# Optimization experiments

Measured on AMD Instinct MI355X. Metric: run time of the kernel, lower is better.

The kernel has to match this reference:

```python
import jax, jax.numpy as jnp
import numpy as np

B, N, NUM = 16384, 512, 3  # batch, num queries, num vanishing points per image


def setup_inputs() -> dict:
    key = jax.random.key(0)
    k1, k2, k3 = jax.random.split(key, 3)
    pred_logits = jax.random.normal(k1, (B, N, 1), jnp.float32)
    pp = jax.random.normal(k2, (B, N, 3), jnp.float32)
    pred_pos = pp / jnp.linalg.norm(pp, axis=-1, keepdims=True)  # unit directions
    vp = jax.random.normal(k3, (B, 3, NUM), jnp.float32)
    vps_unique = vp / jnp.linalg.norm(vp, axis=1, keepdims=True)  # all columns valid (abs-sum > 1e-5)
    return {"pred_logits": pred_logits, "pred_pos": pred_pos, "vps_unique": vps_unique}


def _greedy_select(conf, pos, num):
    # conf: [N,1], pos: [N,3]; greedy angular NMS keeping `num` candidates.
    order = jnp.argsort(-conf[:, 0]).astype(jnp.int32)  # descending confidence
    thresh = jnp.pi / (num + 1)
    ar = jnp.arange(num)
    cand0 = jnp.zeros((num,), jnp.int32).at[0].set(order[0])

    def step(carry, idx):
        cand, count = carry
        sel = pos[cand]                                   # [num,3]
        dots = jnp.minimum(jnp.abs(sel @ pos[idx]), 1.0)  # clip for arccos stability
        ang = jnp.where(ar < count, jnp.arccos(dots), jnp.inf)
        add = (count < num) & (jnp.min(ang) >= thresh)    # torch: skip if dst < pi/(num+1)
        cand = jnp.where(add & (ar == count), idx, cand)
        return (cand, count + add.astype(jnp.int32)), None

    (cand, _), _ = jax.lax.scan(step, (cand0, jnp.int32(1)), order[1:])
    return pos[cand]  # [num,3]


def reference(pred_logits, pred_pos, vps_unique):
    num = vps_unique.shape[2]  # static: all vps columns are valid by construction
    sel = jax.vmap(lambda c, p: _greedy_select(c, p, num))(pred_logits, pred_pos)
    return sel  # [B, num, 3]
```

## Files before the change

### kernel.cpp

```cpp
#include <hip/hip_runtime.h>
#include <math.h>

#define B_TOTAL 16384
#define NQ 512
#define NUM 3
#define TOPK 8

__global__ __launch_bounds__(256) void greedy_nms_kernel(
    const float* __restrict__ conf,
    const float* __restrict__ pos,
    float* __restrict__ out)
{
    const int lane = threadIdx.x & 63;
    const int b = (blockIdx.x << 2) | (threadIdx.x >> 6);

    const float* cb = conf + (size_t)b * NQ;
    const float* pb = pos  + (size_t)b * NQ * 3;

    const float4* cb4 = reinterpret_cast<const float4*>(cb);
    float4 c0 = cb4[lane * 2 + 0];
    float4 c1 = cb4[lane * 2 + 1];
    const float p0x = pb[0], p0y = pb[1], p0z = pb[2];

    unsigned k[8];
    {
        float f[8] = {c0.x, c0.y, c0.z, c0.w, c1.x, c1.y, c1.z, c1.w};
        #pragma unroll
        for (int s = 0; s < 8; ++s) {
            int bi = __float_as_int(f[s]);
            k[s] = (unsigned)bi ^ ((unsigned)(bi >> 31) | 0x80000000u);
        }
    }

    auto argmax64 = [&]() -> unsigned long long {
        bool s01 = k[1] > k[0];
        unsigned m01 = s01 ? k[1] : k[0]; int i01 = s01 ? 1 : 0;
        bool s23 = k[3] > k[2];
        unsigned m23 = s23 ? k[3] : k[2]; int i23 = s23 ? 3 : 2;
        bool s45 = k[5] > k[4];
        unsigned m45 = s45 ? k[5] : k[4]; int i45 = s45 ? 5 : 4;
        bool s67 = k[7] > k[6];
        unsigned m67 = s67 ? k[7] : k[6]; int i67 = s67 ? 7 : 6;
        if (m23 > m01) { m01 = m23; i01 = i23; }
        if (m67 > m45) { m45 = m67; i45 = i67; }
        if (m45 > m01) { m01 = m45; i01 = i45; }
        unsigned long long key =
            ((unsigned long long)m01 << 32) |
            (unsigned)(NQ - 1 - ((lane << 3) + i01));
        #pragma unroll
        for (int off = 1; off < 64; off <<= 1) {
            unsigned long long o = __shfl_xor(key, off);
            if (o > key) key = o;
        }
        return key;
    };

    auto consume = [&](int n) {
        const int osl = ((n >> 3) == lane) ? (n & 7) : 8;
        #pragma unroll
        for (int s = 0; s < 8; ++s)
            if (osl == s) k[s] = 0u;
    };

    int myw = 0;
    #pragma unroll
    for (int i = 0; i < TOPK; ++i) {
        unsigned long long K = argmax64();
        const int n = NQ - 1 - (int)(K & 0x1ffu);
        if (lane == i) myw = n;
        consume(n);
    }

    float cx = pb[myw * 3 + 0];
    float cy = pb[myw * 3 + 1];
    float cz = pb[myw * 3 + 2];

    const float TH  = 0.78539816339744830961f;
    const float CLO = 0.70710478f;
    const float CHI = 0.70710878f;

    auto pass1 = [&](float ax, float ay, float az,
                     float px, float py, float pz) -> bool {
        float d = fabsf(ax * px + ay * py + az * pz);
        if (d <= CLO) return true;
        if (d >= CHI) return false;
        return acosf(fminf(d, 1.f)) >= TH;
    };

    const float p1x = __shfl(cx, 0), p1y = __shfl(cy, 0), p1z = __shfl(cz, 0);
    unsigned long long ball1 =
        __ballot(pass1(p1x, p1y, p1z, cx, cy, cz)) & 0xFEull;

    float o2x = p0x, o2y = p0y, o2z = p0z;
    float o3x = p0x, o3y = p0y, o3z = p0z;
    bool need_fallback;
    float a1x = 0.f, a1y = 0.f, a1z = 0.f;
    int count = 1;

    if (ball1 != 0) {
        const int i2 = __ffsll(ball1) - 1;
        const float p2x = __shfl(cx, i2), p2y = __shfl(cy, i2),
                    p2z = __shfl(cz, i2);
        o2x = p2x; o2y = p2y; o2z = p2z;
        a1x = p2x; a1y = p2y; a1z = p2z;
        count = 2;
        unsigned long long ball3 =
            ball1 & __ballot(pass1(p2x, p2y, p2z, cx, cy, cz))
                  & ~((2ull << i2) - 1);
        if (ball3 != 0) {
            const int i3 = __ffsll(ball3) - 1;
            o3x = __shfl(cx, i3); o3y = __shfl(cy, i3); o3z = __shfl(cz, i3);
            need_fallback = false;
        } else {
            need_fallback = true;
        }
    } else {
        need_fallback = true;
    }

    if (need_fallback) {
        #pragma unroll 1
        for (int it = TOPK; it < NQ; ++it) {
            unsigned long long K = argmax64();
            if ((unsigned)(K >> 32) == 0u) break;
            const int n = NQ - 1 - (int)(K & 0x1ffu);
            consume(n);
            const float px = pb[n * 3 + 0];
            const float py = pb[n * 3 + 1];
            const float pz = pb[n * 3 + 2];
            bool add = pass1(p1x, p1y, p1z, px, py, pz) &&
                       pass1(a1x, a1y, a1z, px, py, pz);
            if (add) {
                if (count == 1) {
                    o2x = px; o2y = py; o2z = pz;
                    a1x = px; a1y = py; a1z = pz;
                    count = 2;
                } else {
                    o3x = px; o3y = py; o3z = pz;
                    break;
                }
            }
        }
    }

    if (lane == 0) {
        float* ob = out + (size_t)b * 9;
        ob[0] = p1x; ob[1] = p1y; ob[2] = p1z;
        ob[3] = o2x; ob[4] = o2y; ob[5] = o2z;
        ob[6] = o3x; ob[7] = o3y; ob[8] = o3z;
    }
}

extern "C" void kernel_launch(void* const* d_in, const int* in_sizes, int n_in,
                              void* d_out, int out_size, void* d_ws, size_t ws_size,
                              hipStream_t stream) {
    const float* pred_logits = (const float*)d_in[0];
    const float* pred_pos    = (const float*)d_in[1];
    float* out = (float*)d_out;

    const int grid = B_TOTAL / 4;
    greedy_nms_kernel<<<grid, 256, 0, stream>>>(pred_logits, pred_pos, out);
}
```

Before: 32.52 us.

## Replace iterative top-8 argmax with bitonic-merge top-8 across the wavefront

Each lane sorts its 8 packed (score, index) keys with a sorting network. Six xor-shuffle stages then merge pairs of sorted 8-lists, keeping the top 8, so every lane holds the wavefront's global top 8. This replaces eight sequential 64-lane argmax reductions, each with 6 dependent shuffles, with 6 stages of 8 parallel 64-bit shuffles and compare-swaps. The common case then exits early after the two ballot tests, and the sequential fallback runs only when the top 8 does not yield three picks. In exchange it uses more registers and issues more shuffle instructions in total.

```diff
diff --git a/kernel.cpp b/kernel.cpp
--- a/kernel.cpp
+++ b/kernel.cpp
@@ -4,7 +4,8 @@
 #define B_TOTAL 16384
 #define NQ 512
 #define NUM 3
-#define TOPK 8
+
+typedef unsigned long long u64;
 
 __global__ __launch_bounds__(256) void greedy_nms_kernel(
     const float* __restrict__ conf,
@@ -20,19 +21,118 @@
     const float4* cb4 = reinterpret_cast<const float4*>(cb);
     float4 c0 = cb4[lane * 2 + 0];
     float4 c1 = cb4[lane * 2 + 1];
+
+    u64 s[8];
+    {
+        float f[8] = {c0.x, c0.y, c0.z, c0.w, c1.x, c1.y, c1.z, c1.w};
+        #pragma unroll
+        for (int i = 0; i < 8; ++i) {
+            int bi = __float_as_int(f[i]);
+            unsigned u = (unsigned)bi ^ ((unsigned)(bi >> 31) | 0x80000000u);
+            s[i] = ((u64)u << 32) | (unsigned)(NQ - 1 - ((lane << 3) + i));
+        }
+    }
+
+    #define CSW(a, c) { if ((c) > (a)) { u64 t_ = (a); (a) = (c); (c) = t_; } }
+
+    CSW(s[0],s[1]) CSW(s[2],s[3]) CSW(s[4],s[5]) CSW(s[6],s[7])
+    CSW(s[0],s[2]) CSW(s[1],s[3]) CSW(s[4],s[6]) CSW(s[5],s[7])
+    CSW(s[1],s[2]) CSW(s[5],s[6])
+    CSW(s[0],s[4]) CSW(s[1],s[5]) CSW(s[2],s[6]) CSW(s[3],s[7])
+    CSW(s[2],s[4]) CSW(s[3],s[5])
+    CSW(s[1],s[2]) CSW(s[3],s[4]) CSW(s[5],s[6])
+
+    #pragma unroll
+    for (int off = 1; off < 64; off <<= 1) {
+        u64 o[8];
+        #pragma unroll
+        for (int i = 0; i < 8; ++i) o[i] = __shfl_xor(s[i], off);
+        u64 m[8];
+        #pragma unroll
+        for (int i = 0; i < 8; ++i) {
+            u64 x = o[7 - i];
+            m[i] = s[i] > x ? s[i] : x;
+        }
+        CSW(m[0],m[4]) CSW(m[1],m[5]) CSW(m[2],m[6]) CSW(m[3],m[7])
+        CSW(m[0],m[2]) CSW(m[1],m[3]) CSW(m[4],m[6]) CSW(m[5],m[7])
+        CSW(m[0],m[1]) CSW(m[2],m[3]) CSW(m[4],m[5]) CSW(m[6],m[7])
+        #pragma unroll
+        for (int i = 0; i < 8; ++i) s[i] = m[i];
+    }
+
+    int myn = NQ - 1 - (int)(s[0] & 0x1ffu);
+    #pragma unroll
+    for (int i = 1; i < 8; ++i)
+        if (lane == i) myn = NQ - 1 - (int)(s[i] & 0x1ffu);
+    float cx = pb[myn * 3 + 0];
+    float cy = pb[myn * 3 + 1];
+    float cz = pb[myn * 3 + 2];
+
+    const float TH  = 0.78539816339744830961f;
+    const float CLO = 0.70710478f;
+    const float CHI = 0.70710878f;
+
+    auto passv = [&](float ax, float ay, float az,
+                     float px, float py, float pz) -> bool {
+        float d = fabsf(ax * px + ay * py + az * pz);
+        if (d <= CLO) return true;
+        if (d >= CHI) return false;
+        return acosf(fminf(d, 1.f)) >= TH;
+    };
+
+    const float p1x = __shfl(cx, 0), p1y = __shfl(cy, 0), p1z = __shfl(cz, 0);
+    u64 ball1 = __ballot(passv(p1x, p1y, p1z, cx, cy, cz)) & 0xFEull;
+
+    float o2x, o2y, o2z;
+    const bool found2 = (ball1 != 0);
+    if (found2) {
+        const int i2 = __ffsll(ball1) - 1;
+        o2x = __shfl(cx, i2); o2y = __shfl(cy, i2); o2z = __shfl(cz, i2);
+        u64 ball3 = ball1 & __ballot(passv(o2x, o2y, o2z, cx, cy, cz))
+                          & ~((2ull << i2) - 1);
+        if (ball3 != 0) {
+            const int i3 = __ffsll(ball3) - 1;
+            const float o3x = __shfl(cx, i3);
+            const float o3y = __shfl(cy, i3);
+            const float o3z = __shfl(cz, i3);
+            if (lane == 0) {
+                float* ob = out + (size_t)b * 9;
+                ob[0] = p1x; ob[1] = p1y; ob[2] = p1z;
+                ob[3] = o2x; ob[4] = o2y; ob[5] = o2z;
+                ob[6] = o3x; ob[7] = o3y; ob[8] = o3z;
+            }
+            return;
+        }
+    }
+
     const float p0x = pb[0], p0y = pb[1], p0z = pb[2];
 
     unsigned k[8];
     {
         float f[8] = {c0.x, c0.y, c0.z, c0.w, c1.x, c1.y, c1.z, c1.w};
         #pragma unroll
-        for (int s = 0; s < 8; ++s) {
-            int bi = __float_as_int(f[s]);
-            k[s] = (unsigned)bi ^ ((unsigned)(bi >> 31) | 0x80000000u);
+        for (int i = 0; i < 8; ++i) {
+            int bi = __float_as_int(f[i]);
+            k[i] = (unsigned)bi ^ ((unsigned)(bi >> 31) | 0x80000000u);
         }
     }
+    #pragma unroll
+    for (int r = 0; r < 8; ++r) {
+        const int nr = NQ - 1 - (int)(s[r] & 0x1ffu);
+        const int osl = ((nr >> 3) == lane) ? (nr & 7) : 8;
+        #pragma unroll
+        for (int q = 0; q < 8; ++q)
+            if (osl == q) k[q] = 0u;
+    }
 
-    auto argmax64 = [&]() -> unsigned long long {
+    float a1x = 0.f, a1y = 0.f, a1z = 0.f;
+    float o3x = p0x, o3y = p0y, o3z = p0z;
+    int count;
+    if (found2) { a1x = o2x; a1y = o2y; a1z = o2z; count = 2; }
+    else        { o2x = p0x; o2y = p0y; o2z = p0z; count = 1; }
+
+    #pragma unroll 1
+    for (int it = 8; it < NQ; ++it) {
         bool s01 = k[1] > k[0];
         unsigned m01 = s01 ? k[1] : k[0]; int i01 = s01 ? 1 : 0;
         bool s23 = k[3] > k[2];
@@ -44,101 +144,34 @@
         if (m23 > m01) { m01 = m23; i01 = i23; }
         if (m67 > m45) { m45 = m67; i45 = i67; }
         if (m45 > m01) { m01 = m45; i01 = i45; }
-        unsigned long long key =
-            ((unsigned long long)m01 << 32) |
-            (unsigned)(NQ - 1 - ((lane << 3) + i01));
+        u64 K = ((u64)m01 << 32) |
+                (unsigned)(NQ - 1 - ((lane << 3) + i01));
         #pragma unroll
         for (int off = 1; off < 64; off <<= 1) {
-            unsigned long long o = __shfl_xor(key, off);
-            if (o > key) key = o;
+            u64 o = __shfl_xor(K, off);
+            if (o > K) K = o;
         }
-        return key;
-    };
-
-    auto consume = [&](int n) {
-        const int osl = ((n >> 3) == lane) ? (n & 7) : 8;
-        #pragma unroll
-        for (int s = 0; s < 8; ++s)
-            if (osl == s) k[s] = 0u;
-    };
-
-    int myw = 0;
-    #pragma unroll
-    for (int i = 0; i < TOPK; ++i) {
-        unsigned long long K = argmax64();
+        if ((unsigned)(K >> 32) == 0u) break;
         const int n = NQ - 1 - (int)(K & 0x1ffu);
-        if (lane == i) myw = n;
-        consume(n);
-    }
-
-    float cx = pb[myw * 3 + 0];
-    float cy = pb[myw * 3 + 1];
-    float cz = pb[myw * 3 + 2];
-
-    const float TH  = 0.78539816339744830961f;
-    const float CLO = 0.70710478f;
-    const float CHI = 0.70710878f;
-
-    auto pass1 = [&](float ax, float ay, float az,
-                     float px, float py, float pz) -> bool {
-        float d = fabsf(ax * px + ay * py + az * pz);
-        if (d <= CLO) return true;
-        if (d >= CHI) return false;
-        return acosf(fminf(d, 1.f)) >= TH;
-    };
-
-    const float p1x = __shfl(cx, 0), p1y = __shfl(cy, 0), p1z = __shfl(cz, 0);
-    unsigned long long ball1 =
-        __ballot(pass1(p1x, p1y, p1z, cx, cy, cz)) & 0xFEull;
-
-    float o2x = p0x, o2y = p0y, o2z = p0z;
-    float o3x = p0x, o3y = p0y, o3z = p0z;
-    bool need_fallback;
-    float a1x = 0.f, a1y = 0.f, a1z = 0.f;
-    int count = 1;
-
-    if (ball1 != 0) {
-        const int i2 = __ffsll(ball1) - 1;
-        const float p2x = __shfl(cx, i2), p2y = __shfl(cy, i2),
-                    p2z = __shfl(cz, i2);
-        o2x = p2x; o2y = p2y; o2z = p2z;
-        a1x = p2x; a1y = p2y; a1z = p2z;
-        count = 2;
-        unsigned long long ball3 =
-            ball1 & __ballot(pass1(p2x, p2y, p2z, cx, cy, cz))
-                  & ~((2ull << i2) - 1);
-        if (ball3 != 0) {
-            const int i3 = __ffsll(ball3) - 1;
-            o3x = __shfl(cx, i3); o3y = __shfl(cy, i3); o3z = __shfl(cz, i3);
-            need_fallback = false;
-        } else {
-            need_fallback = true;
+        {
+            const int osl = ((n >> 3) == lane) ? (n & 7) : 8;
+            #pragma unroll
+            for (int q = 0; q < 8; ++q)
+                if (osl == q) k[q] = 0u;
         }
-    } else {
-        need_fallback = true;
-    }
-
-    if (need_fallback) {
-        #pragma unroll 1
-        for (int it = TOPK; it < NQ; ++it) {
-            unsigned long long K = argmax64();
-            if ((unsigned)(K >> 32) == 0u) break;
-            const int n = NQ - 1 - (int)(K & 0x1ffu);
-            consume(n);
-            const float px = pb[n * 3 + 0];
-            const float py = pb[n * 3 + 1];
-            const float pz = pb[n * 3 + 2];
-            bool add = pass1(p1x, p1y, p1z, px, py, pz) &&
-                       pass1(a1x, a1y, a1z, px, py, pz);
-            if (add) {
-                if (count == 1) {
-                    o2x = px; o2y = py; o2z = pz;
-                    a1x = px; a1y = py; a1z = pz;
-                    count = 2;
-                } else {
-                    o3x = px; o3y = py; o3z = pz;
-                    break;
-                }
+        const float px = pb[n * 3 + 0];
+        const float py = pb[n * 3 + 1];
+        const float pz = pb[n * 3 + 2];
+        bool add = passv(p1x, p1y, p1z, px, py, pz) &&
+                   passv(a1x, a1y, a1z, px, py, pz);
+        if (add) {
+            if (count == 1) {
+                o2x = px; o2y = py; o2z = pz;
+                a1x = px; a1y = py; a1z = pz;
+                count = 2;
+            } else {
+                o3x = px; o3y = py; o3z = pz;
+                break;
             }
         }
     }
```

Result: slower. 42.81 us (+31.6%).
